# Optimization experiments

Measured on AMD Instinct MI355X. Metric: run time of the kernel, lower is better.

Reference implementation:

```python
import jax, jax.numpy as jnp
import numpy as np

B, S, D, H, DQK, DH = 2, 2048, 1024, 16, 64, 64

def setup_inputs() -> dict:
    key = jax.random.key(0)
    ks = jax.random.split(key, 9)
    return {
        "x":  jax.random.normal(ks[0], (B, S, D), jnp.float32),
        "Wq": jax.random.normal(ks[1], (H, D, DQK), jnp.float32) * (D ** -0.5),
        "bq": jax.random.normal(ks[2], (H, DQK), jnp.float32) * 0.02,
        "Wk": jax.random.normal(ks[3], (H, D, DQK), jnp.float32) * (D ** -0.5),
        "bk": jax.random.normal(ks[4], (H, DQK), jnp.float32) * 0.02,
        "Wv": jax.random.normal(ks[5], (H, D, DH), jnp.float32) * (D ** -0.5),
        "bv": jax.random.normal(ks[6], (H, DH), jnp.float32) * 0.02,
        "Wo": jax.random.normal(ks[7], (D, D), jnp.float32) * (D ** -0.5),
        "bo": jax.random.normal(ks[8], (D,), jnp.float32) * 0.02,
    }

def reference(x, Wq, bq, Wk, bk, Wv, bv, Wo, bo):
    b, s, d = x.shape
    # per-head projections, all heads batched: [B,H,S,*]
    Q = jnp.einsum('bsd,hde->bhse', x, Wq) + bq[None, :, None, :]
    K = jnp.einsum('bsd,hde->bhse', x, Wk) + bk[None, :, None, :]
    V = jnp.einsum('bsd,hde->bhse', x, Wv) + bv[None, :, None, :]
    scores = jnp.einsum('bhse,bhte->bhst', Q, K) * (Q.shape[-1] ** -0.5)
    causal = jnp.tril(jnp.ones((s, s), bool))
    scores = jnp.where(causal, scores, -jnp.inf)  # mask add as in torch code
    attn = jax.nn.softmax(scores, axis=-1)        # dropout p=0 (eval)
    out = jnp.einsum('bhst,bhtd->bhsd', attn, V)
    # concat heads along feature dim (head order matches torch.cat)
    out = out.transpose(0, 2, 1, 3).reshape(b, s, -1)
    return out @ Wo + bo
```

## Files before the change

### kernel.cpp

```cpp
#include <hip/hip_runtime.h>
#include <stdint.h>

typedef __attribute__((ext_vector_type(8))) short bh8;
typedef __attribute__((ext_vector_type(4))) float f32x4;
typedef __attribute__((ext_vector_type(4))) unsigned short u16x4;
typedef __attribute__((ext_vector_type(8))) unsigned short u16x8;
typedef __attribute__((ext_vector_type(2))) unsigned int u32x2;

#define DEVI static __device__ __forceinline__

constexpr int B_ = 2, S_ = 2048, D_ = 1024, H_ = 16, E_ = 64;

constexpr size_t OFF_XB  = 0;
constexpr size_t OFF_WQT = OFF_XB  + (size_t)B_*S_*D_;
constexpr size_t OFF_WKT = OFF_WQT + (size_t)H_*E_*D_;
constexpr size_t OFF_WVT = OFF_WKT + (size_t)H_*E_*D_;
constexpr size_t OFF_WOT = OFF_WVT + (size_t)H_*E_*D_;
constexpr size_t OFF_Q   = OFF_WOT + (size_t)D_*D_;
constexpr size_t OFF_K   = OFF_Q   + (size_t)B_*H_*S_*E_;
constexpr size_t OFF_VT  = OFF_K   + (size_t)B_*H_*S_*E_;
constexpr size_t OFF_O   = OFF_VT  + (size_t)B_*H_*S_*E_;

DEVI unsigned short f2bf(float f) {
    union { float f; unsigned u; } v; v.f = f;
    unsigned u = v.u;
    return (unsigned short)((u + 0x7fffu + ((u >> 16) & 1u)) >> 16);
}

DEVI unsigned cvt_pk_bf16(float lo, float hi) {
    unsigned r;
    asm("v_cvt_pk_bf16_f32 %0, %1, %2" : "=v"(r) : "v"(lo), "v"(hi));
    return r;
}

DEVI void gload16(const void* g, void* l) {
    __builtin_amdgcn_global_load_lds(
        (const __attribute__((address_space(1))) unsigned int*)g,
        (__attribute__((address_space(3))) unsigned int*)l, 16, 0, 0);
}

DEVI f32x4 mfma16(bh8 a, bh8 b, f32x4 c) {
    return __builtin_amdgcn_mfma_f32_16x16x32_bf16(a, b, c, 0, 0, 0);
}

template<int N> DEVI void vm_barrier() {
    asm volatile("s_waitcnt vmcnt(%0)" :: "i"(N) : "memory");
    __builtin_amdgcn_s_barrier();
    __builtin_amdgcn_sched_barrier(0);
}
DEVI void post_barrier() {
    __builtin_amdgcn_sched_barrier(0);
    __builtin_amdgcn_s_barrier();
    __builtin_amdgcn_sched_barrier(0);
}

__global__ __launch_bounds__(256) void k_convert_x(const float* __restrict__ x,
                                                   unsigned short* __restrict__ ws) {
    const int i = blockIdx.x * 256 + threadIdx.x;
    const float4 v = ((const float4*)x)[i];
    u16x4 o = { f2bf(v.x), f2bf(v.y), f2bf(v.z), f2bf(v.w) };
    *(u16x4*)(ws + OFF_XB + (size_t)i * 4) = o;
}

__global__ __launch_bounds__(256) void k_transpose_w(const float* __restrict__ Wq,
                                                     const float* __restrict__ Wk,
                                                     const float* __restrict__ Wv,
                                                     const float* __restrict__ Wo,
                                                     unsigned short* __restrict__ ws) {
    const int xi = blockIdx.x;
    const int z  = blockIdx.y;
    const int t  = threadIdx.x;
    __shared__ __align__(16) unsigned short tile[64][72];

    const float* src; unsigned short* dst;
    int inCols, inBase, outBase;
    if (z < 3) {
        src = (z == 0) ? Wq : (z == 1) ? Wk : Wv;
        dst = ws + ((z == 0) ? OFF_WQT : (z == 1) ? OFF_WKT : OFF_WVT);
        inCols = 64;
        inBase = xi * 64 * 64;
        const int h = xi >> 4, dt = xi & 15;
        outBase = h * 65536 + dt * 64;
    } else {
        src = Wo; dst = ws + OFF_WOT;
        inCols = 1024;
        const int et = xi >> 4, dt = xi & 15;
        inBase  = (dt * 64) * 1024 + et * 64;
        outBase = (et * 64) * 1024 + dt * 64;
    }
#pragma unroll
    for (int v = 0; v < 4; ++v) {
        const int flat = v * 256 + t;
        const int i = flat >> 4, j4 = (flat & 15) * 4;
        const float4 val = *(const float4*)(src + inBase + i * inCols + j4);
        tile[i][j4 + 0] = f2bf(val.x);
        tile[i][j4 + 1] = f2bf(val.y);
        tile[i][j4 + 2] = f2bf(val.z);
        tile[i][j4 + 3] = f2bf(val.w);
    }
    __syncthreads();
    const int j = t >> 2, iseg = (t & 3) * 16;
    u16x8 p0, p1;
#pragma unroll
    for (int u = 0; u < 8; ++u) p0[u] = tile[iseg + u][j];
#pragma unroll
    for (int u = 0; u < 8; ++u) p1[u] = tile[iseg + 8 + u][j];
    *(u16x8*)(dst + outBase + (size_t)j * 1024 + iseg)     = p0;
    *(u16x8*)(dst + outBase + (size_t)j * 1024 + iseg + 8) = p1;
}

DEVI void gemm_tile_128x128(const unsigned short* __restrict__ A,
                            const unsigned short* __restrict__ Bw,
                            unsigned short* lds,
                            f32x4 acc[2][8]) {
    const int lane = threadIdx.x & 63;
    const int w    = threadIdx.x >> 6;
    const int lr = lane & 15, lg = lane >> 4;
    const unsigned short* a0 = A  + (size_t)((w * 2 + 0) * 16 + lr) * D_ + lg * 8;
    const unsigned short* a1 = A  + (size_t)((w * 2 + 1) * 16 + lr) * D_ + lg * 8;
    const unsigned short* b0 = Bw + (size_t)((w * 2 + 0) * 16 + lr) * D_ + lg * 8;
    const unsigned short* b1 = Bw + (size_t)((w * 2 + 1) * 16 + lr) * D_ + lg * 8;
    const int oA0 = (w * 2 + 0) * 512, oA1 = (w * 2 + 1) * 512;
    const int oB0 = 4096 + oA0,        oB1 = 4096 + oA1;

    auto stage = [&](int ks, int bufi) {
        unsigned short* base = lds + bufi * 8192;
        gload16(a0 + ks * 32, base + oA0);
        gload16(a1 + ks * 32, base + oA1);
        gload16(b0 + ks * 32, base + oB0);
        gload16(b1 + ks * 32, base + oB1);
    };

    stage(0, 0); stage(1, 1);
    for (int ks = 0; ks < 32; ++ks) {
        if (ks < 31) vm_barrier<4>();
        else         vm_barrier<0>();
        if (ks + 2 < 32) stage(ks + 2, (ks + 2) % 3);
        const unsigned short* base = lds + (ks % 3) * 8192;
        bh8 af0 = *(const bh8*)(base + (w * 2 + 0) * 512 + lane * 8);
        bh8 af1 = *(const bh8*)(base + (w * 2 + 1) * 512 + lane * 8);
#pragma unroll
        for (int nt = 0; nt < 8; ++nt) {
            bh8 bf = *(const bh8*)(base + 4096 + nt * 512 + lane * 8);
            acc[0][nt] = mfma16(af0, bf, acc[0][nt]);
            acc[1][nt] = mfma16(af1, bf, acc[1][nt]);
        }
        __builtin_amdgcn_sched_barrier(0);
    }
}

__global__ __launch_bounds__(256, 3) void k_qkv(unsigned short* __restrict__ ws,
                                                const float* __restrict__ bq,
                                                const float* __restrict__ bk,
                                                const float* __restrict__ bv) {
    const int flat  = blockIdx.x;
    const int idx   = flat >> 3;
    const int stile = (flat & 7) * 4 + (idx & 3);
    const int ntile = idx >> 2;
    const int row0  = stile * 128;
    const unsigned short* A  = ws + OFF_XB  + (size_t)row0 * D_;
    const unsigned short* Bw = ws + OFF_WQT + (size_t)ntile * 128 * D_;

    __shared__ __align__(16) unsigned short lds[3 * 8192];
    f32x4 acc[2][8];
#pragma unroll
    for (int i = 0; i < 2; ++i)
#pragma unroll
        for (int j = 0; j < 8; ++j) acc[i][j] = (f32x4){0.f, 0.f, 0.f, 0.f};

    gemm_tile_128x128(A, Bw, lds, acc);

    const int lane = threadIdx.x & 63, w = threadIdx.x >> 6;
    const int lr = lane & 15, lg = lane >> 4;
    const int srow0 = row0 + w * 32;
    const int b     = srow0 >> 11;
    const int sl0   = srow0 & (S_ - 1);
#pragma unroll
    for (int mt = 0; mt < 2; ++mt) {
#pragma unroll
        for (int nt = 0; nt < 8; ++nt) {
            const int gcol = ntile * 128 + nt * 16;
            const int mat  = gcol >> 10;
            const int h    = (gcol >> 6) & 15;
            const int e    = (gcol & 63) + lr;
            const int bh   = b * H_ + h;
            const float bia = ((mat == 0) ? bq : (mat == 1) ? bk : bv)[h * 64 + e];
            if (mat == 0) {
                u16x4 pk;
#pragma unroll
                for (int r = 0; r < 4; ++r)
                    pk[r] = f2bf((acc[mt][nt][r] + bia) * 0.1803368801f);
                const int sl = sl0 + mt * 16 + lg * 4;
                *(u16x4*)(ws + OFF_Q + ((size_t)(bh * E_ + e)) * S_ + sl) = pk;
            } else if (mat == 2) {
                u16x4 pk;
#pragma unroll
                for (int r = 0; r < 4; ++r) pk[r] = f2bf(acc[mt][nt][r] + bia);
                const int sl = sl0 + mt * 16 + lg * 4;
                *(u16x4*)(ws + OFF_VT + ((size_t)(bh * E_ + e)) * S_ + sl) = pk;
            } else {
#pragma unroll
                for (int r = 0; r < 4; ++r) {
                    const int sl = sl0 + mt * 16 + lg * 4 + r;
                    ws[OFF_K + ((size_t)bh * S_ + sl) * E_ + e] = f2bf(acc[mt][nt][r] + bia);
                }
            }
        }
    }
}

__global__ __launch_bounds__(256, 4) void k_attn(unsigned short* __restrict__ ws) {
    const int flat = blockIdx.x;
    const int j    = flat & 31;
    const int qt   = 31 - (flat >> 5);
    const int bh   = (j & 7) * 4 + (j >> 3);
    const int lane = threadIdx.x & 63, w = threadIdx.x >> 6;
    const int lr = lane & 15, lg = lane >> 4;
    const unsigned short* Qp = ws + OFF_Q  + (size_t)bh * E_ * S_;
    const unsigned short* Kp = ws + OFF_K  + (size_t)bh * S_ * E_;
    const unsigned short* Vp = ws + OFF_VT + (size_t)bh * E_ * S_;
    __shared__ __align__(16) unsigned short ldsK[2][8 * 512];
    __shared__ __align__(16) unsigned short ldsV[2][8 * 512];
    __shared__ __align__(16) unsigned short ldsP[4 * 1024];

    const int qbase = qt * 64 + w * 16;
    bh8 qf[2];
#pragma unroll
    for (int kg = 0; kg < 2; ++kg) {
        bh8 t;
#pragma unroll
        for (int i = 0; i < 8; ++i)
            t[i] = (short)Qp[(size_t)(kg * 32 + lg * 8 + i) * S_ + qbase + lr];
        qf[kg] = t;
    }

    f32x4 o[4];
    float m = -3.0e38f, l = 0.f;
#pragma unroll
    for (int i = 0; i < 4; ++i) o[i] = (f32x4){0.f, 0.f, 0.f, 0.f};

    auto stage = [&](int kt, int bufi) {
        const int sk0 = kt * 64;
#pragma unroll
        for (int u = 0; u < 2; ++u) {
            const int blk = w * 2 + u;
            const int ct = blk >> 1, kg = blk & 1;
            gload16(Kp + (size_t)(sk0 + ct * 16 + lr) * E_ + kg * 32 + lg * 8,
                    &ldsK[bufi][blk * 512]);
            gload16(Vp + (size_t)(ct * 16 + lr) * S_ + sk0 + kg * 32 + lg * 8,
                    &ldsV[bufi][blk * 512]);
        }
    };

    unsigned short* Pw = ldsP + w * 1024;

    stage(0, 0);
    if (qt >= 1) stage(1, 1);

    for (int kt = 0; kt <= qt; ++kt) {
        if (kt < qt) vm_barrier<4>();
        else         vm_barrier<0>();
        const int cur = kt & 1;
        const unsigned short* Kc = ldsK[cur];
        const unsigned short* Vc = ldsV[cur];

        f32x4 sc[4];
#pragma unroll
        for (int ct = 0; ct < 4; ++ct) sc[ct] = (f32x4){0.f, 0.f, 0.f, 0.f};
#pragma unroll
        for (int ct = 0; ct < 4; ++ct)
#pragma unroll
            for (int kg = 0; kg < 2; ++kg) {
                bh8 kf = *(const bh8*)(Kc + (ct * 2 + kg) * 512 + lane * 8);
                sc[ct] = mfma16(kf, qf[kg], sc[ct]);
            }
        if (kt == qt) {
#pragma unroll
            for (int ct = 0; ct < 4; ++ct) {
                const int skl = ct * 16 + lg * 4;
#pragma unroll
                for (int r = 0; r < 4; ++r)
                    if (skl + r > w * 16 + lr) sc[ct][r] = -3.0e38f;
            }
        }
        float mx = fmaxf(fmaxf(sc[0][0], sc[0][1]), fmaxf(sc[0][2], sc[0][3]));
#pragma unroll
        for (int ct = 1; ct < 4; ++ct)
            mx = fmaxf(mx, fmaxf(fmaxf(sc[ct][0], sc[ct][1]),
                                 fmaxf(sc[ct][2], sc[ct][3])));
        mx = fmaxf(mx, __shfl_xor(mx, 16, 64));
        mx = fmaxf(mx, __shfl_xor(mx, 32, 64));
        const bool need = mx > m + 8.0f;
        if (__any(need)) {
            const float mn = need ? mx : m;
            const float sf = __builtin_amdgcn_exp2f(m - mn);
            m = mn;
            l *= sf;
#pragma unroll
            for (int r = 0; r < 4; ++r) {
                const float sfq = __shfl(sf, (lane & 48) + lg * 4 + r, 64);
#pragma unroll
                for (int et = 0; et < 4; ++et) o[et][r] *= sfq;
            }
        }
        float rs = 0.f;
#pragma unroll
        for (int ct = 0; ct < 4; ++ct)
#pragma unroll
            for (int r = 0; r < 4; ++r) {
                float p = __builtin_amdgcn_exp2f(sc[ct][r] - m);
                sc[ct][r] = p;
                rs += p;
            }
        rs += __shfl_xor(rs, 16, 64);
        rs += __shfl_xor(rs, 32, 64);
        l += rs;
#pragma unroll
        for (int ct = 0; ct < 4; ++ct) {
            u32x2 pk = { cvt_pk_bf16(sc[ct][0], sc[ct][1]),
                         cvt_pk_bf16(sc[ct][2], sc[ct][3]) };
            const int addr = (ct >> 1) * 512 +
                             ((((ct & 1) * 2) + (lg >> 1)) * 16 + lr) * 8 + (lg & 1) * 4;
            *(u32x2*)(Pw + addr) = pk;
        }
#pragma unroll
        for (int skg = 0; skg < 2; ++skg) {
            bh8 pf = *(const bh8*)(Pw + skg * 512 + lane * 8);
#pragma unroll
            for (int et = 0; et < 4; ++et) {
                bh8 vf = *(const bh8*)(Vc + (et * 2 + skg) * 512 + lane * 8);
                o[et] = mfma16(pf, vf, o[et]);
            }
        }
        post_barrier();
        if (kt + 2 <= qt) stage(kt + 2, cur);
    }
    const int b = bh >> 4, hh = bh & 15;
#pragma unroll
    for (int r = 0; r < 4; ++r) {
        const float lq = __shfl(l, (lane & 48) + lg * 4 + r, 64);
        const float inv = 1.0f / lq;
        const int s = qbase + lg * 4 + r;
#pragma unroll
        for (int et = 0; et < 4; ++et)
            ws[OFF_O + ((size_t)(b * S_ + s)) * D_ + hh * E_ + et * 16 + lr] =
                f2bf(o[et][r] * inv);
    }
}

__global__ __launch_bounds__(256, 3) void k_oproj(const unsigned short* __restrict__ ws,
                                                  const float* __restrict__ bo,
                                                  float* __restrict__ out) {
    const int flat  = blockIdx.x;
    const int idx   = flat >> 3;
    const int stile = (flat & 7) * 4 + (idx & 3);
    const int ntile = idx >> 2;
    const unsigned short* A  = ws + OFF_O   + (size_t)stile * 128 * D_;
    const unsigned short* Bw = ws + OFF_WOT + (size_t)ntile * 128 * D_;
    __shared__ __align__(16) unsigned short lds[3 * 8192];
    f32x4 acc[2][8];
#pragma unroll
    for (int i = 0; i < 2; ++i)
#pragma unroll
        for (int j = 0; j < 8; ++j) acc[i][j] = (f32x4){0.f, 0.f, 0.f, 0.f};

    gemm_tile_128x128(A, Bw, lds, acc);

    const int lane = threadIdx.x & 63, w = threadIdx.x >> 6;
    const int lr = lane & 15, lg = lane >> 4;
    const int r0 = stile * 128 + w * 32;
#pragma unroll
    for (int mt = 0; mt < 2; ++mt)
#pragma unroll
        for (int nt = 0; nt < 8; ++nt) {
            const int e = ntile * 128 + nt * 16 + lr;
            const float bia = bo[e];
#pragma unroll
            for (int r = 0; r < 4; ++r)
                out[(size_t)(r0 + mt * 16 + lg * 4 + r) * D_ + e] = acc[mt][nt][r] + bia;
        }
}

extern "C" void kernel_launch(void* const* d_in, const int* in_sizes, int n_in,
                              void* d_out, int out_size, void* d_ws, size_t ws_size,
                              hipStream_t stream) {
    const float* x  = (const float*)d_in[0];
    const float* Wq = (const float*)d_in[1];
    const float* bq = (const float*)d_in[2];
    const float* Wk = (const float*)d_in[3];
    const float* bk = (const float*)d_in[4];
    const float* Wv = (const float*)d_in[5];
    const float* bv = (const float*)d_in[6];
    const float* Wo = (const float*)d_in[7];
    const float* bo = (const float*)d_in[8];
    float* out = (float*)d_out;
    unsigned short* ws = (unsigned short*)d_ws;

    k_convert_x<<<dim3((B_ * S_ * D_) / 4 / 256), 256, 0, stream>>>(x, ws);
    k_transpose_w<<<dim3(256, 4), 256, 0, stream>>>(Wq, Wk, Wv, Wo, ws);
    k_qkv<<<dim3(768), 256, 0, stream>>>(ws, bq, bk, bv);
    k_attn<<<dim3(1024), 256, 0, stream>>>(ws);
    k_oproj<<<dim3(256), 256, 0, stream>>>(ws, bo, out);
}
```

Measured before the change: 128.8 us.

## Split long causal query tiles across two KV-range blocks and merge partials

The upper 16 query tiles of causal attention are each split into two blocks covering halves of the key range, each writing unnormalized partial outputs plus running max and sum to workspace (reusing the x-bf16 region). A new merge kernel combines the two partials with rescaled softmax statistics and writes the final head output. This is meant to shorten the critical path of the longest blocks and balance load across CUs. In exchange it adds an extra launch, extra global traffic for the partials, and bf16 rounding of the unnormalized partial outputs.

```diff
diff --git a/kernel.cpp b/kernel.cpp
--- a/kernel.cpp
+++ b/kernel.cpp
@@ -20,11 +20,16 @@
 constexpr size_t OFF_K   = OFF_Q   + (size_t)B_*H_*S_*E_;
 constexpr size_t OFF_VT  = OFF_K   + (size_t)B_*H_*S_*E_;
 constexpr size_t OFF_O   = OFF_VT  + (size_t)B_*H_*S_*E_;
+constexpr size_t OFF_PO  = OFF_XB;
+constexpr size_t OFF_PML = OFF_XB + 4*1024*1024;
 
 DEVI unsigned short f2bf(float f) {
     union { float f; unsigned u; } v; v.f = f;
     unsigned u = v.u;
     return (unsigned short)((u + 0x7fffu + ((u >> 16) & 1u)) >> 16);
+}
+DEVI float bf2f(unsigned short u) {
+    union { unsigned u; float f; } v; v.u = (unsigned)u << 16; return v.f;
 }
 
 DEVI unsigned cvt_pk_bf16(float lo, float hi) {
@@ -211,9 +216,22 @@
 
 __global__ __launch_bounds__(256, 4) void k_attn(unsigned short* __restrict__ ws) {
     const int flat = blockIdx.x;
-    const int j    = flat & 31;
-    const int qt   = 31 - (flat >> 5);
-    const int bh   = (j & 7) * 4 + (j >> 3);
+    int qt, j, kt_begin, kt_end, part;
+    if (flat < 1024) {
+        const int s = flat & 511;
+        part = flat >> 9;
+        qt = 31 - (s >> 5);
+        j  = s & 31;
+        const int h = (qt + 2) >> 1;
+        kt_begin = part ? h : 0;
+        kt_end   = part ? qt + 1 : h;
+    } else {
+        const int s2 = flat - 1024;
+        qt = 15 - (s2 >> 5);
+        j  = s2 & 31;
+        kt_begin = 0; kt_end = qt + 1; part = -1;
+    }
+    const int bh = (j & 7) * 4 + (j >> 3);
     const int lane = threadIdx.x & 63, w = threadIdx.x >> 6;
     const int lr = lane & 15, lg = lane >> 4;
     const unsigned short* Qp = ws + OFF_Q  + (size_t)bh * E_ * S_;
@@ -254,13 +272,13 @@
 
     unsigned short* Pw = ldsP + w * 1024;
 
-    stage(0, 0);
-    if (qt >= 1) stage(1, 1);
-
-    for (int kt = 0; kt <= qt; ++kt) {
-        if (kt < qt) vm_barrier<4>();
-        else         vm_barrier<0>();
-        const int cur = kt & 1;
+    stage(kt_begin, 0);
+    if (kt_begin + 1 < kt_end) stage(kt_begin + 1, 1);
+
+    for (int kt = kt_begin; kt < kt_end; ++kt) {
+        if (kt + 1 < kt_end) vm_barrier<4>();
+        else                 vm_barrier<0>();
+        const int cur = (kt - kt_begin) & 1;
         const unsigned short* Kc = ldsK[cur];
         const unsigned short* Vc = ldsV[cur];
 
@@ -333,19 +351,73 @@
             }
         }
         post_barrier();
-        if (kt + 2 <= qt) stage(kt + 2, cur);
+        if (kt + 2 < kt_end) stage(kt + 2, cur);
+    }
+    if (part < 0) {
+        const int b = bh >> 4, hh = bh & 15;
+#pragma unroll
+        for (int r = 0; r < 4; ++r) {
+            const float lq = __shfl(l, (lane & 48) + lg * 4 + r, 64);
+            const float inv = 1.0f / lq;
+            const int s = qbase + lg * 4 + r;
+#pragma unroll
+            for (int et = 0; et < 4; ++et)
+                ws[OFF_O + ((size_t)(b * S_ + s)) * D_ + hh * E_ + et * 16 + lr] =
+                    f2bf(o[et][r] * inv);
+        }
+    } else {
+        const int p = ((qt - 16) * 32 + bh) * 2 + part;
+        unsigned short* Op = ws + OFF_PO + (size_t)p * 4096;
+        float* mlb = (float*)(ws + OFF_PML) + p * 128;
+#pragma unroll
+        for (int r = 0; r < 4; ++r) {
+            const int row = w * 16 + lg * 4 + r;
+#pragma unroll
+            for (int et = 0; et < 4; ++et)
+                Op[row * 64 + et * 16 + lr] = f2bf(o[et][r]);
+        }
+        if (lg == 0) {
+            mlb[(w * 16 + lr) * 2]     = m;
+            mlb[(w * 16 + lr) * 2 + 1] = l;
+        }
+    }
+}
+
+__global__ __launch_bounds__(256) void k_merge(unsigned short* __restrict__ ws) {
+    const int qi = blockIdx.x >> 5;
+    const int qt = 16 + qi;
+    const int j  = blockIdx.x & 31;
+    const int bh = (j & 7) * 4 + (j >> 3);
+    const int p0 = ((qt - 16) * 32 + bh) * 2;
+    const unsigned short* Oa = ws + OFF_PO + (size_t)p0 * 4096;
+    const unsigned short* Ob = Oa + 4096;
+    const float* mla = (const float*)(ws + OFF_PML) + p0 * 128;
+    const float* mlb = mla + 128;
+
+    const int t = threadIdx.x;
+    const int row = t >> 2, cg = t & 3;
+    const float ma = mla[row * 2], la = mla[row * 2 + 1];
+    const float mb = mlb[row * 2], lb = mlb[row * 2 + 1];
+    const float mm = fmaxf(ma, mb);
+    const float sa = __builtin_amdgcn_exp2f(ma - mm);
+    const float sb = __builtin_amdgcn_exp2f(mb - mm);
+    const float inv = 1.0f / (la * sa + lb * sb);
+
+    u16x8 va0 = *(const u16x8*)(Oa + row * 64 + cg * 16);
+    u16x8 va1 = *(const u16x8*)(Oa + row * 64 + cg * 16 + 8);
+    u16x8 vb0 = *(const u16x8*)(Ob + row * 64 + cg * 16);
+    u16x8 vb1 = *(const u16x8*)(Ob + row * 64 + cg * 16 + 8);
+    u16x8 o0, o1;
+#pragma unroll
+    for (int i = 0; i < 8; ++i) {
+        o0[i] = f2bf((bf2f(va0[i]) * sa + bf2f(vb0[i]) * sb) * inv);
+        o1[i] = f2bf((bf2f(va1[i]) * sa + bf2f(vb1[i]) * sb) * inv);
     }
     const int b = bh >> 4, hh = bh & 15;
-#pragma unroll
-    for (int r = 0; r < 4; ++r) {
-        const float lq = __shfl(l, (lane & 48) + lg * 4 + r, 64);
-        const float inv = 1.0f / lq;
-        const int s = qbase + lg * 4 + r;
-#pragma unroll
-        for (int et = 0; et < 4; ++et)
-            ws[OFF_O + ((size_t)(b * S_ + s)) * D_ + hh * E_ + et * 16 + lr] =
-                f2bf(o[et][r] * inv);
-    }
+    const int s = qt * 64 + row;
+    unsigned short* dst = ws + OFF_O + ((size_t)(b * S_ + s)) * D_ + hh * E_ + cg * 16;
+    *(u16x8*)(dst)     = o0;
+    *(u16x8*)(dst + 8) = o1;
 }
 
 __global__ __launch_bounds__(256, 3) void k_oproj(const unsigned short* __restrict__ ws,
@@ -399,6 +471,7 @@
     k_convert_x<<<dim3((B_ * S_ * D_) / 4 / 256), 256, 0, stream>>>(x, ws);
     k_transpose_w<<<dim3(256, 4), 256, 0, stream>>>(Wq, Wk, Wv, Wo, ws);
     k_qkv<<<dim3(768), 256, 0, stream>>>(ws, bq, bk, bv);
-    k_attn<<<dim3(1024), 256, 0, stream>>>(ws);
+    k_attn<<<dim3(1536), 256, 0, stream>>>(ws);
+    k_merge<<<dim3(512), 256, 0, stream>>>(ws);
     k_oproj<<<dim3(256), 256, 0, stream>>>(ws, bo, out);
 }
```

Measured after the change: 130.7 us. No clear change (+1.5%).

## Rewrite QKV GEMM as 256x256 tiles with 8 waves and split-phase pipelining

Applied to the files above, without the earlier changes.

Replaces the 128x128 QKV projection kernel (768 blocks of 256 threads) with 256x256 tiles computed by 512-thread blocks (192 blocks). Each wave handles a 128x64 sub-tile, loading K in 64-wide double-buffered slices and interleaving the global-to-LDS loads between four MFMA phases, with s_setprio raised around the MFMA bursts. The aim is to raise arithmetic intensity per LDS byte and hide load latency better. In exchange it uses 128 KB of LDS and only 192 blocks, which may leave some of the 256 CUs idle.

```diff
diff --git a/kernel.cpp b/kernel.cpp
--- a/kernel.cpp
+++ b/kernel.cpp
@@ -109,6 +109,164 @@
     *(u16x8*)(dst + outBase + (size_t)j * 1024 + iseg + 8) = p1;
 }
 
+DEVI void qkv_stA(const unsigned short* Ap, unsigned short* lds, int kt, int mh, int ks,
+                  int lane, int w, int lr, int lg) {
+    const int b = kt & 1;
+    const int mfrag = (w >> 2) * 8 + mh * 4 + (w & 3);
+    gload16(Ap + (size_t)(mfrag * 16 + lr) * D_ + kt * 64 + ks * 32 + lg * 8,
+            lds + b * 16384 + (mfrag * 2 + ks) * 512 + lane * 8);
+}
+DEVI void qkv_stB(const unsigned short* Bp, unsigned short* lds, int kt, int ks,
+                  int lane, int w, int lr, int lg) {
+    const int b = kt & 1;
+#pragma unroll
+    for (int u = 0; u < 2; ++u) {
+        const int nfrag = w * 2 + u;
+        gload16(Bp + (size_t)(nfrag * 16 + lr) * D_ + kt * 64 + ks * 32 + lg * 8,
+                lds + 32768 + b * 16384 + (nfrag * 2 + ks) * 512 + lane * 8);
+    }
+}
+DEVI bh8 qkv_ldA(const unsigned short* lds, int b, int mfrag, int ks, int lane) {
+    return *(const bh8*)(lds + b * 16384 + (mfrag * 2 + ks) * 512 + lane * 8);
+}
+DEVI bh8 qkv_ldB(const unsigned short* lds, int b, int nfrag, int ks, int lane) {
+    return *(const bh8*)(lds + 32768 + b * 16384 + (nfrag * 2 + ks) * 512 + lane * 8);
+}
+
+template<int V0, int V1, int V2, int V3, bool S0, bool S123>
+DEVI void qkv_ktile(int kt, const unsigned short* Ap, const unsigned short* Bp,
+                    unsigned short* lds, int lane, int w, int lr, int lg,
+                    int wm, int wn, f32x4 (&acc)[8][4]) {
+    const int b = kt & 1;
+    bh8 af[4], bf[4];
+    vm_barrier<V0>();
+#pragma unroll
+    for (int n = 0; n < 4; ++n) bf[n] = qkv_ldB(lds, b, wn * 4 + n, 0, lane);
+#pragma unroll
+    for (int q = 0; q < 4; ++q) af[q] = qkv_ldA(lds, b, wm * 8 + q, 0, lane);
+    if (S0) qkv_stA(Ap, lds, kt + 1, 1, 1, lane, w, lr, lg);
+    __builtin_amdgcn_s_setprio(1);
+#pragma unroll
+    for (int q = 0; q < 4; ++q)
+#pragma unroll
+        for (int n = 0; n < 4; ++n) acc[q][n] = mfma16(af[q], bf[n], acc[q][n]);
+    __builtin_amdgcn_s_setprio(0);
+    __builtin_amdgcn_sched_barrier(0);
+    vm_barrier<V1>();
+#pragma unroll
+    for (int q = 0; q < 4; ++q) af[q] = qkv_ldA(lds, b, wm * 8 + 4 + q, 0, lane);
+    if (S123) {
+        qkv_stA(Ap, lds, kt + 2, 0, 0, lane, w, lr, lg);
+        qkv_stB(Bp, lds, kt + 2, 0, lane, w, lr, lg);
+    }
+    __builtin_amdgcn_s_setprio(1);
+#pragma unroll
+    for (int q = 0; q < 4; ++q)
+#pragma unroll
+        for (int n = 0; n < 4; ++n) acc[4 + q][n] = mfma16(af[q], bf[n], acc[4 + q][n]);
+    __builtin_amdgcn_s_setprio(0);
+    __builtin_amdgcn_sched_barrier(0);
+    vm_barrier<V2>();
+#pragma unroll
+    for (int n = 0; n < 4; ++n) bf[n] = qkv_ldB(lds, b, wn * 4 + n, 1, lane);
+#pragma unroll
+    for (int q = 0; q < 4; ++q) af[q] = qkv_ldA(lds, b, wm * 8 + q, 1, lane);
+    if (S123) qkv_stA(Ap, lds, kt + 2, 1, 0, lane, w, lr, lg);
+    __builtin_amdgcn_s_setprio(1);
+#pragma unroll
+    for (int q = 0; q < 4; ++q)
+#pragma unroll
+        for (int n = 0; n < 4; ++n) acc[q][n] = mfma16(af[q], bf[n], acc[q][n]);
+    __builtin_amdgcn_s_setprio(0);
+    __builtin_amdgcn_sched_barrier(0);
+    vm_barrier<V3>();
+#pragma unroll
+    for (int q = 0; q < 4; ++q) af[q] = qkv_ldA(lds, b, wm * 8 + 4 + q, 1, lane);
+    if (S123) {
+        qkv_stA(Ap, lds, kt + 2, 0, 1, lane, w, lr, lg);
+        qkv_stB(Bp, lds, kt + 2, 1, lane, w, lr, lg);
+    }
+    __builtin_amdgcn_s_setprio(1);
+#pragma unroll
+    for (int q = 0; q < 4; ++q)
+#pragma unroll
+        for (int n = 0; n < 4; ++n) acc[4 + q][n] = mfma16(af[q], bf[n], acc[4 + q][n]);
+    __builtin_amdgcn_s_setprio(0);
+    __builtin_amdgcn_sched_barrier(0);
+}
+
+__global__ __launch_bounds__(512, 2) void k_qkv(unsigned short* __restrict__ ws,
+                                                const float* __restrict__ bq,
+                                                const float* __restrict__ bk,
+                                                const float* __restrict__ bv) {
+    const int flat  = blockIdx.x;
+    const int idx   = flat >> 3;
+    const int stile = (flat & 7) * 2 + (idx & 1);
+    const int ntile = idx >> 1;
+    const unsigned short* Ap = ws + OFF_XB  + (size_t)stile * 256 * D_;
+    const unsigned short* Bp = ws + OFF_WQT + (size_t)ntile * 256 * D_;
+
+    __shared__ __align__(16) unsigned short lds[65536];
+    const int tid = threadIdx.x, lane = tid & 63, w = tid >> 6;
+    const int lr = lane & 15, lg = lane >> 4;
+    const int wm = w >> 2, wn = w & 3;
+
+    f32x4 acc[8][4];
+#pragma unroll
+    for (int i = 0; i < 8; ++i)
+#pragma unroll
+        for (int j = 0; j < 4; ++j) acc[i][j] = (f32x4){0.f, 0.f, 0.f, 0.f};
+
+    qkv_stA(Ap, lds, 0, 0, 0, lane, w, lr, lg);
+    qkv_stB(Bp, lds, 0, 0, lane, w, lr, lg);
+    qkv_stA(Ap, lds, 0, 1, 0, lane, w, lr, lg);
+    qkv_stA(Ap, lds, 0, 0, 1, lane, w, lr, lg);
+    qkv_stB(Bp, lds, 0, 1, lane, w, lr, lg);
+    qkv_stA(Ap, lds, 0, 1, 1, lane, w, lr, lg);
+    qkv_stA(Ap, lds, 1, 0, 0, lane, w, lr, lg);
+    qkv_stB(Bp, lds, 1, 0, lane, w, lr, lg);
+    qkv_stA(Ap, lds, 1, 1, 0, lane, w, lr, lg);
+    qkv_stA(Ap, lds, 1, 0, 1, lane, w, lr, lg);
+    qkv_stB(Bp, lds, 1, 1, lane, w, lr, lg);
+
+    for (int kt = 0; kt < 14; ++kt)
+        qkv_ktile<12, 12, 12, 12, true, true>(kt, Ap, Bp, lds, lane, w, lr, lg, wm, wn, acc);
+    qkv_ktile<12, 12, 9, 8, true, false>(14, Ap, Bp, lds, lane, w, lr, lg, wm, wn, acc);
+    qkv_ktile<5, 4, 1, 0, false, false>(15, Ap, Bp, lds, lane, w, lr, lg, wm, wn, acc);
+
+    const int c = ntile * 4 + wn;
+    const int mat = c >> 4, h = c & 15;
+    const float* bias = ((mat == 0) ? bq : (mat == 1) ? bk : bv) + h * 64;
+    const int bb = stile >> 3;
+    const int bh = bb * H_ + h;
+#pragma unroll
+    for (int mf = 0; mf < 8; ++mf) {
+        const int sl = ((stile * 256 + wm * 128 + mf * 16) & (S_ - 1)) + lg * 4;
+#pragma unroll
+        for (int nf = 0; nf < 4; ++nf) {
+            const int e = nf * 16 + lr;
+            const float bia = bias[e];
+            if (mat == 0) {
+                u16x4 pk;
+#pragma unroll
+                for (int r = 0; r < 4; ++r)
+                    pk[r] = f2bf((acc[mf][nf][r] + bia) * 0.1803368801f);
+                *(u16x4*)(ws + OFF_Q + ((size_t)(bh * E_ + e)) * S_ + sl) = pk;
+            } else if (mat == 2) {
+                u16x4 pk;
+#pragma unroll
+                for (int r = 0; r < 4; ++r) pk[r] = f2bf(acc[mf][nf][r] + bia);
+                *(u16x4*)(ws + OFF_VT + ((size_t)(bh * E_ + e)) * S_ + sl) = pk;
+            } else {
+#pragma unroll
+                for (int r = 0; r < 4; ++r)
+                    ws[OFF_K + ((size_t)bh * S_ + sl + r) * E_ + e] =
+                        f2bf(acc[mf][nf][r] + bia);
+            }
+        }
+    }
+}
+
 DEVI void gemm_tile_128x128(const unsigned short* __restrict__ A,
                             const unsigned short* __restrict__ Bw,
                             unsigned short* lds,
@@ -146,66 +304,6 @@
             acc[1][nt] = mfma16(af1, bf, acc[1][nt]);
         }
         __builtin_amdgcn_sched_barrier(0);
-    }
-}
-
-__global__ __launch_bounds__(256, 3) void k_qkv(unsigned short* __restrict__ ws,
-                                                const float* __restrict__ bq,
-                                                const float* __restrict__ bk,
-                                                const float* __restrict__ bv) {
-    const int flat  = blockIdx.x;
-    const int idx   = flat >> 3;
-    const int stile = (flat & 7) * 4 + (idx & 3);
-    const int ntile = idx >> 2;
-    const int row0  = stile * 128;
-    const unsigned short* A  = ws + OFF_XB  + (size_t)row0 * D_;
-    const unsigned short* Bw = ws + OFF_WQT + (size_t)ntile * 128 * D_;
-
-    __shared__ __align__(16) unsigned short lds[3 * 8192];
-    f32x4 acc[2][8];
-#pragma unroll
-    for (int i = 0; i < 2; ++i)
-#pragma unroll
-        for (int j = 0; j < 8; ++j) acc[i][j] = (f32x4){0.f, 0.f, 0.f, 0.f};
-
-    gemm_tile_128x128(A, Bw, lds, acc);
-
-    const int lane = threadIdx.x & 63, w = threadIdx.x >> 6;
-    const int lr = lane & 15, lg = lane >> 4;
-    const int srow0 = row0 + w * 32;
-    const int b     = srow0 >> 11;
-    const int sl0   = srow0 & (S_ - 1);
-#pragma unroll
-    for (int mt = 0; mt < 2; ++mt) {
-#pragma unroll
-        for (int nt = 0; nt < 8; ++nt) {
-            const int gcol = ntile * 128 + nt * 16;
-            const int mat  = gcol >> 10;
-            const int h    = (gcol >> 6) & 15;
-            const int e    = (gcol & 63) + lr;
-            const int bh   = b * H_ + h;
-            const float bia = ((mat == 0) ? bq : (mat == 1) ? bk : bv)[h * 64 + e];
-            if (mat == 0) {
-                u16x4 pk;
-#pragma unroll
-                for (int r = 0; r < 4; ++r)
-                    pk[r] = f2bf((acc[mt][nt][r] + bia) * 0.1803368801f);
-                const int sl = sl0 + mt * 16 + lg * 4;
-                *(u16x4*)(ws + OFF_Q + ((size_t)(bh * E_ + e)) * S_ + sl) = pk;
-            } else if (mat == 2) {
-                u16x4 pk;
-#pragma unroll
-                for (int r = 0; r < 4; ++r) pk[r] = f2bf(acc[mt][nt][r] + bia);
-                const int sl = sl0 + mt * 16 + lg * 4;
-                *(u16x4*)(ws + OFF_VT + ((size_t)(bh * E_ + e)) * S_ + sl) = pk;
-            } else {
-#pragma unroll
-                for (int r = 0; r < 4; ++r) {
-                    const int sl = sl0 + mt * 16 + lg * 4 + r;
-                    ws[OFF_K + ((size_t)bh * S_ + sl) * E_ + e] = f2bf(acc[mt][nt][r] + bia);
-                }
-            }
-        }
     }
 }
 
@@ -398,7 +496,7 @@
 
     k_convert_x<<<dim3((B_ * S_ * D_) / 4 / 256), 256, 0, stream>>>(x, ws);
     k_transpose_w<<<dim3(256, 4), 256, 0, stream>>>(Wq, Wk, Wv, Wo, ws);
-    k_qkv<<<dim3(768), 256, 0, stream>>>(ws, bq, bk, bv);
+    k_qkv<<<dim3(192), 512, 0, stream>>>(ws, bq, bk, bv);
     k_attn<<<dim3(1024), 256, 0, stream>>>(ws);
     k_oproj<<<dim3(256), 256, 0, stream>>>(ws, bo, out);
 }
```

After: 118.9 us. 1.08x faster.
